# Kernel tuning notes

Hardware: AMD Instinct MI355X
Metric: run time of the kernel (lower is better)

The kernel has to match this reference:

```python
import jax, jax.numpy as jnp
import numpy as np

B, LQ, LK, D, H, DK, DV = 8, 1024, 1024, 512, 8, 64, 64
EPS = 1e-14          # K.epsilon()**2 with default K.epsilon()=1e-7
MASK_VALUE = -1e30   # default mask_value in call()


def setup_inputs() -> dict:
    key = jax.random.key(0)
    ks = jax.random.split(key, 7)
    query = jax.random.normal(ks[0], (B, LQ, D), jnp.float32)
    key_t = jax.random.normal(ks[1], (B, LK, D), jnp.float32)
    value = jax.random.normal(ks[2], (B, LK, D), jnp.float32)
    mask = jax.random.randint(ks[3], (B, LK), 0, 2).astype(jnp.float32)
    glorot = np.sqrt(2.0 / (D + DK)).astype(np.float32)
    Wq = jax.random.normal(ks[4], (H, D, DK), jnp.float32) * glorot
    Wk = jax.random.normal(ks[5], (H, D, DK), jnp.float32) * glorot
    Wv = jax.random.normal(ks[6], (H, D, DV), jnp.float32) * glorot
    gamma = jnp.ones((1,), jnp.float32)
    beta = jnp.zeros((1,), jnp.float32)
    return {"query": query, "key": key_t, "value": value, "mask": mask,
            "Wq": Wq, "Wk": Wk, "Wv": Wv, "gamma": gamma, "beta": beta}


def reference(query, key, value, mask, Wq, Wk, Wv, gamma, beta):
    # Per-head projections (the original's Python loop over heads, vectorized).
    q = jnp.einsum('bqd,hde->bhqe', query, Wq)   # [B,H,LQ,DK]
    k = jnp.einsum('bkd,hde->bhke', key, Wk)     # [B,H,LK,DK]
    v = jnp.einsum('bkd,hde->bhke', value, Wv)   # [B,H,LK,DV]
    # NOTE: no 1/sqrt(dk) scaling, faithful to the source.
    A = jnp.einsum('bhqe,bhke->bhqk', q, k)      # [B,H,LQ,LK]
    m = mask[:, None, None, :]                    # [B,1,1,LK] broadcast over heads & queries
    A = m * A + (1.0 - m) * MASK_VALUE
    A = jax.nn.softmax(A, axis=-1)
    o = jnp.einsum('bhqk,bhke->bhqe', A, v)      # [B,H,LQ,DV]
    conc = o.transpose(0, 2, 1, 3).reshape(B, LQ, H * DV)  # concat heads
    # Scalar-affine layernorm over the concatenated feature dim.
    mean = jnp.mean(conc, axis=-1, keepdims=True)
    var = jnp.mean(jnp.square(conc - mean), axis=-1, keepdims=True)
    x = (conc - mean) / jnp.sqrt(var + EPS)
    return x * gamma[0] + beta[0]
```

## Files before the change

### kernel.cpp

```cpp
#include <hip/hip_runtime.h>
#include <math.h>

#define NB 8
#define NLQ 1024
#define NLK 1024
#define ND 512
#define NH 8
#define MASKV -1e30f
#define LOG2E 1.44269504088896f
#define SHIFT2 32.0f

typedef unsigned short ushort_t;
typedef __attribute__((ext_vector_type(8))) _Float16 f16x8;
typedef __attribute__((ext_vector_type(8))) short bf16x8;
typedef __attribute__((ext_vector_type(16))) float f32x16;

__device__ __forceinline__ ushort_t f2h_bits(float f) {
    union { _Float16 h; ushort_t u; } v; v.h = (_Float16)f;
    return v.u;
}
__device__ __forceinline__ ushort_t f2bf(float f) {
    union { float f; unsigned u; } v; v.f = f;
    unsigned r = v.u + 0x7fffu + ((v.u >> 16) & 1u);
    return (ushort_t)(r >> 16);
}
__device__ __forceinline__ void gload16(const ushort_t* g, ushort_t* l) {
    __builtin_amdgcn_global_load_lds(
        (const __attribute__((address_space(1))) void*)g,
        (__attribute__((address_space(3))) void*)l, 16, 0, 0);
}
__device__ __forceinline__ void gload16f(const float* g, float* l) {
    __builtin_amdgcn_global_load_lds(
        (const __attribute__((address_space(1))) void*)g,
        (__attribute__((address_space(3))) void*)l, 16, 0, 0);
}
__device__ __forceinline__ unsigned pack_bf16_trunc(float p0, float p1) {
    return __builtin_amdgcn_perm(__float_as_uint(p1), __float_as_uint(p0),
                                 0x07060302u);
}

__global__ __launch_bounds__(256) void wsplit_kernel(
    const float* __restrict__ Wq, const float* __restrict__ Wk, const float* __restrict__ Wv,
    ushort_t* __restrict__ oq, ushort_t* __restrict__ ok, ushort_t* __restrict__ ov) {
    __shared__ float T[64][65];
    const int d0 = blockIdx.x * 64;
    const int h  = blockIdx.y;
    const int t  = blockIdx.z;
    const float* W = (t == 0) ? Wq : (t == 1) ? Wk : Wv;
    ushort_t* oh = (t == 0) ? oq : (t == 1) ? ok : ov;
    const int tid = threadIdx.x;
#pragma unroll
    for (int i = 0; i < 4; i++) {
        int r = (tid >> 4) + i * 16;
        int c = (tid & 15) * 4;
        float4 v = *(const float4*)&W[((size_t)h * ND + d0 + r) * 64 + c];
        *(float4*)&T[r][c] = v;
    }
    __syncthreads();
    const int e = tid & 63;
    const int dg = tid >> 6;
    ushort_t hs[16];
#pragma unroll
    for (int dd = 0; dd < 16; dd++) hs[dd] = f2h_bits(T[dg * 16 + dd][e]);
    size_t base = ((size_t)h * 64 + e) * ND + d0 + dg * 16;
#pragma unroll
    for (int c = 0; c < 2; c++) {
        uint4 wh;
        wh.x = (unsigned)hs[8*c+0] | ((unsigned)hs[8*c+1] << 16);
        wh.y = (unsigned)hs[8*c+2] | ((unsigned)hs[8*c+3] << 16);
        wh.z = (unsigned)hs[8*c+4] | ((unsigned)hs[8*c+5] << 16);
        wh.w = (unsigned)hs[8*c+6] | ((unsigned)hs[8*c+7] << 16);
        *(uint4*)&oh[base + 8 * c] = wh;
    }
}

__global__ __launch_bounds__(256, 3) void proj_mfma_kernel(
    const float* __restrict__ Xq, const float* __restrict__ Xk,
    const float* __restrict__ Xv, const ushort_t* __restrict__ Wbase,
    ushort_t* __restrict__ Obase) {
    __shared__ float    sXf[2][4160];
    __shared__ ushort_t sW [2][4160];

    const int l0 = blockIdx.x * 64;
    const int h  = blockIdx.y;
    const int z  = blockIdx.z;
    const int t  = z >> 3;
    const int b  = z & 7;
    const int tid  = threadIdx.x;
    const int wave = tid >> 6;
    const int lane = tid & 63;
    const int l31  = lane & 31;
    const int hib  = lane >> 5;
    const size_t bh = (size_t)b * NH + h;

    const float* Xt = (t == 0) ? Xq : (t == 1) ? Xk : Xv;
    const float* gx = Xt + ((size_t)b * NLQ + l0) * ND;
    const ushort_t* gw = Wbase + (size_t)t * ((size_t)NH * 64 * ND)
                       + (size_t)h * 64 * ND;
    ushort_t* out = Obase + (size_t)t * ((size_t)NB * NH * NLQ * 64);

    const int srow = lane >> 3;
    const int schk = (lane & 7) ^ srow;
    const int xrow = lane >> 4;
    const int xc16 = lane & 15;

    auto stage = [&](int buf, int d0) {
#pragma unroll
        for (int j = 0; j < 4; j++) {
            int s = j * 4 + wave;
            int row = s * 4 + xrow;
            int c16 = xc16 ^ ((row & 7) << 1);
            gload16f(gx + (size_t)row * ND + d0 + c16 * 4, sXf[buf] + s * 260);
        }
#pragma unroll
        for (int i = 0; i < 2; i++) {
            int u = i * 4 + wave;
            int row = u * 8 + srow;
            gload16(gw + (size_t)row * ND + d0 + schk * 8, sW[buf] + u * 520);
        }
    };

    f32x16 acc;
#pragma unroll
    for (int i = 0; i < 16; i++) acc[i] = 0.f;

    const int arow  = (wave >> 1) * 32 + l31;
    const int brow  = (wave & 1) * 32 + l31;
    const int xbase = (arow >> 2) * 260 + (arow & 3) * 64;
    const int sxz   = (arow & 7) << 1;
    const int bpad  = (brow >> 3) * 520 + (brow & 7) * 64;
    const int sw    = l31 & 7;

    stage(0, 0);
    int cur = 0;
#pragma unroll
    for (int kc = 0; kc < 8; kc++) {
        if (kc < 7) {
            stage(cur ^ 1, (kc + 1) * 64);
            asm volatile("s_waitcnt vmcnt(6)" ::: "memory");
        } else {
            asm volatile("s_waitcnt vmcnt(0)" ::: "memory");
        }
        __builtin_amdgcn_sched_barrier(0);
        __builtin_amdgcn_s_barrier();
        __builtin_amdgcn_sched_barrier(0);
#pragma unroll
        for (int c = 0; c < 4; c++) {
            const int sl = ((2 * c + hib) * 2) ^ sxz;
            const float* xp = &sXf[cur][xbase + sl * 4];
            float4 fa = *(const float4*)xp;
            float4 fb = *(const float4*)(xp + 4);
            f16x8 xh;
            xh[0] = (_Float16)fa.x; xh[1] = (_Float16)fa.y;
            xh[2] = (_Float16)fa.z; xh[3] = (_Float16)fa.w;
            xh[4] = (_Float16)fb.x; xh[5] = (_Float16)fb.y;
            xh[6] = (_Float16)fb.z; xh[7] = (_Float16)fb.w;
            const int pc = ((2 * c + hib) ^ sw) * 8;
            f16x8 wh = *(const f16x8*)&sW[cur][bpad + pc];
            acc = __builtin_amdgcn_mfma_f32_32x32x16_f16(xh, wh, acc, 0, 0, 0);
        }
        __builtin_amdgcn_sched_barrier(0);
        __builtin_amdgcn_s_barrier();
        __builtin_amdgcn_sched_barrier(0);
        cur ^= 1;
    }

    if (t < 2) {
        const float scale = (t == 0) ? LOG2E : 1.f;
        const size_t obase = (bh * NLQ + l0) * 64;
        const int e = (wave & 1) * 32 + l31;
#pragma unroll
        for (int r = 0; r < 16; r++) {
            int l = (wave >> 1) * 32 + (r & 3) + 8 * (r >> 2) + 4 * hib;
            out[obase + (size_t)l * 64 + e] = f2h_bits(acc[r] * scale);
        }
    } else {
        ushort_t (*T)[68] = (ushort_t(*)[68])sXf;
        const int e = (wave & 1) * 32 + l31;
#pragma unroll
        for (int r = 0; r < 16; r++) {
            int l = (wave >> 1) * 32 + (r & 3) + 8 * (r >> 2) + 4 * hib;
            T[e][l] = f2bf(acc[r]);
        }
        __syncthreads();
        const int e2 = tid >> 2;
        const int lc = (tid & 3) * 16;
        size_t base = (bh * 64 + e2) * NLK + l0 + lc;
        *(uint4*)&out[base]     = *(const uint4*)&T[e2][lc];
        *(uint4*)&out[base + 8] = *(const uint4*)&T[e2][lc + 8];
    }
}

__global__ __launch_bounds__(256, 4) void attn_kernel(
    const ushort_t* __restrict__ Qf, const ushort_t* __restrict__ Kf,
    const ushort_t* __restrict__ Vt, const float* __restrict__ maskp,
    float* __restrict__ Op) {
    __shared__ ushort_t sK[2][4160];
    __shared__ ushort_t sV[2][4160];
    __shared__ float sBias[1024];

    const int idx = blockIdx.x;
    const int bh_i = idx & 63;
    const int qc  = idx >> 6;
    const int b = bh_i >> 3, h = bh_i & 7;
    const size_t bh = (size_t)b * NH + h;

    const int tid  = threadIdx.x;
    const int wave = tid >> 6;
    const int lane = tid & 63;
    const int l31  = lane & 31;
    const int hib  = lane >> 5;
    const int q = qc * 128 + wave * 32 + l31;
    const int sw = l31 & 7;

    {
        const float* mrow = maskp + ((size_t)b << 10);
        float4 m0 = *(const float4*)&mrow[tid * 4];
        float4 bi;
        bi.x = (m0.x > 0.5f) ? -SHIFT2 : MASKV;
        bi.y = (m0.y > 0.5f) ? -SHIFT2 : MASKV;
        bi.z = (m0.z > 0.5f) ? -SHIFT2 : MASKV;
        bi.w = (m0.w > 0.5f) ? -SHIFT2 : MASKV;
        *(float4*)&sBias[tid * 4] = bi;
    }

    f16x8 qh[4];
    {
        const ushort_t* ph = Qf + (bh * NLQ + q) * 64 + hib * 8;
#pragma unroll
        for (int c = 0; c < 4; c++) qh[c] = *(const f16x8*)(ph + c * 16);
    }

    const int srow = lane >> 3;
    const int schk = (lane & 7) ^ srow;

    auto stage = [&](int buf, int k0) {
#pragma unroll
        for (int n = 0; n < 4; n++) {
            int u = wave + n * 4;
            if (u < 8) {
                int row = u * 8 + srow;
                int key = (row & ~12) | ((row & 4) << 1) | ((row & 8) >> 1);
                gload16(Kf + ((bh << 10) + k0 + key) * 64 + schk * 8,
                        sK[buf] + u * 520);
            } else {
                int u8 = u - 8;
                int row = u8 * 8 + srow;
                gload16(Vt + ((bh << 6) + row) * NLK + k0 + schk * 8,
                        sV[buf] + u8 * 520);
            }
        }
    };

    f32x16 O0, O1;
#pragma unroll
    for (int i = 0; i < 16; i++) { O0[i] = 0.f; O1[i] = 0.f; }
    float lrun = 0.f;

    const int rp0 = (l31 >> 3) * 520 + (l31 & 7) * 64;
    const int rp1 = rp0 + 4 * 520;

    stage(0, 0);
    __syncthreads();
    int cur = 0;

    for (int t = 0; t < 16; t++) {
        const int k0 = t << 6;
        if (t < 15) stage(cur ^ 1, k0 + 64);

        f32x16 S0, S1;
#pragma unroll
        for (int g = 0; g < 4; g++) {
            const int kb = k0 + 16 * (g >> 1) + 8 * hib + 4 * (g & 1);
            float4 b0 = *(const float4*)&sBias[kb];
            float4 b1 = *(const float4*)&sBias[kb + 32];
            S0[4 * g + 0] = b0.x; S0[4 * g + 1] = b0.y;
            S0[4 * g + 2] = b0.z; S0[4 * g + 3] = b0.w;
            S1[4 * g + 0] = b1.x; S1[4 * g + 1] = b1.y;
            S1[4 * g + 2] = b1.z; S1[4 * g + 3] = b1.w;
        }
#pragma unroll
        for (int c = 0; c < 4; c++) {
            const int pc = ((2 * c + hib) ^ sw) * 8;
            f16x8 a0 = *(const f16x8*)&sK[cur][rp0 + pc];
            f16x8 a1 = *(const f16x8*)&sK[cur][rp1 + pc];
            S0 = __builtin_amdgcn_mfma_f32_32x32x16_f16(a0, qh[c], S0, 0, 0, 0);
            S1 = __builtin_amdgcn_mfma_f32_32x32x16_f16(a1, qh[c], S1, 0, 0, 0);
        }

        unsigned pq[8][2];
#pragma unroll
        for (int g = 0; g < 8; g++) {
            float p0, p1, p2, p3;
            if (g < 4) {
                p0 = __builtin_amdgcn_exp2f(S0[4*g+0]);
                p1 = __builtin_amdgcn_exp2f(S0[4*g+1]);
                p2 = __builtin_amdgcn_exp2f(S0[4*g+2]);
                p3 = __builtin_amdgcn_exp2f(S0[4*g+3]);
            } else {
                p0 = __builtin_amdgcn_exp2f(S1[4*(g-4)+0]);
                p1 = __builtin_amdgcn_exp2f(S1[4*(g-4)+1]);
                p2 = __builtin_amdgcn_exp2f(S1[4*(g-4)+2]);
                p3 = __builtin_amdgcn_exp2f(S1[4*(g-4)+3]);
            }
            lrun += (p0 + p1) + (p2 + p3);
            pq[g][0] = pack_bf16_trunc(p0, p1);
            pq[g][1] = pack_bf16_trunc(p2, p3);
        }

#pragma unroll
        for (int c = 0; c < 4; c++) {
            union { unsigned u[4]; bf16x8 v; } pf;
            pf.u[0] = pq[2 * c][0];     pf.u[1] = pq[2 * c][1];
            pf.u[2] = pq[2 * c + 1][0]; pf.u[3] = pq[2 * c + 1][1];
            const int pc = ((2 * c + hib) ^ sw) * 8;
            bf16x8 v0 = *(const bf16x8*)&sV[cur][rp0 + pc];
            bf16x8 v1 = *(const bf16x8*)&sV[cur][rp1 + pc];
            O0 = __builtin_amdgcn_mfma_f32_32x32x16_bf16(v0, pf.v, O0, 0, 0, 0);
            O1 = __builtin_amdgcn_mfma_f32_32x32x16_bf16(v1, pf.v, O1, 0, 0, 0);
        }
        __syncthreads();
        cur ^= 1;
    }

    lrun += __shfl_xor(lrun, 32);
    const float linv = 1.f / lrun;
    float* obase = Op + ((size_t)(b * NLQ + q)) * (NH * 64) + h * 64;
#pragma unroll
    for (int me = 0; me < 2; me++) {
#pragma unroll
        for (int g = 0; g < 4; g++) {
            int e0 = me * 32 + 8 * g + 4 * hib;
            float4 o;
            if (me == 0) {
                o.x = O0[4 * g + 0] * linv; o.y = O0[4 * g + 1] * linv;
                o.z = O0[4 * g + 2] * linv; o.w = O0[4 * g + 3] * linv;
            } else {
                o.x = O1[4 * g + 0] * linv; o.y = O1[4 * g + 1] * linv;
                o.z = O1[4 * g + 2] * linv; o.w = O1[4 * g + 3] * linv;
            }
            *(float4*)&obase[e0] = o;
        }
    }
}

__global__ __launch_bounds__(256) void ln_kernel(const float* __restrict__ X,
                                                 const float* __restrict__ gamma,
                                                 const float* __restrict__ beta,
                                                 float* __restrict__ out) {
    const int row = blockIdx.x * 4 + (threadIdx.x >> 6);
    const int lane = threadIdx.x & 63;
    const float* x = &X[(size_t)row * 512];
    float4 v0 = *(const float4*)&x[lane * 8];
    float4 v1 = *(const float4*)&x[lane * 8 + 4];
    float sum = v0.x + v0.y + v0.z + v0.w + v1.x + v1.y + v1.z + v1.w;
    float sq = v0.x * v0.x + v0.y * v0.y + v0.z * v0.z + v0.w * v0.w
             + v1.x * v1.x + v1.y * v1.y + v1.z * v1.z + v1.w * v1.w;
#pragma unroll
    for (int off = 32; off > 0; off >>= 1) {
        sum += __shfl_down(sum, off);
        sq  += __shfl_down(sq, off);
    }
    sum = __shfl(sum, 0);
    sq  = __shfl(sq, 0);
    const float mean = sum * (1.f / 512.f);
    const float var = sq * (1.f / 512.f) - mean * mean;
    const float rstd = rsqrtf(var + 1e-14f);
    const float g = gamma[0], be = beta[0];
    float* o = &out[(size_t)row * 512];
    float4 r0, r1;
    r0.x = (v0.x - mean) * rstd * g + be;  r0.y = (v0.y - mean) * rstd * g + be;
    r0.z = (v0.z - mean) * rstd * g + be;  r0.w = (v0.w - mean) * rstd * g + be;
    r1.x = (v1.x - mean) * rstd * g + be;  r1.y = (v1.y - mean) * rstd * g + be;
    r1.z = (v1.z - mean) * rstd * g + be;  r1.w = (v1.w - mean) * rstd * g + be;
    *(float4*)&o[lane * 8] = r0;
    *(float4*)&o[lane * 8 + 4] = r1;
}

extern "C" void kernel_launch(void* const* d_in, const int* in_sizes, int n_in,
                              void* d_out, int out_size, void* d_ws, size_t ws_size,
                              hipStream_t stream) {
    const float* query = (const float*)d_in[0];
    const float* key_t = (const float*)d_in[1];
    const float* value = (const float*)d_in[2];
    const float* mask  = (const float*)d_in[3];
    const float* Wq    = (const float*)d_in[4];
    const float* Wk    = (const float*)d_in[5];
    const float* Wv    = (const float*)d_in[6];
    const float* gamma = (const float*)d_in[7];
    const float* beta  = (const float*)d_in[8];
    float* out = (float*)d_out;

    const size_t A = (size_t)NB * NLQ * ND;
    const size_t WS = (size_t)NH * 64 * ND;
    ushort_t* Qf = (ushort_t*)d_ws;
    ushort_t* Kf = Qf + A;
    ushort_t* Vt = Qf + 2 * A;
    ushort_t* Wt = Qf + 3 * A;

    wsplit_kernel<<<dim3(ND / 64, NH, 3), 256, 0, stream>>>(
        Wq, Wk, Wv, Wt, Wt + WS, Wt + 2 * WS);

    proj_mfma_kernel<<<dim3(NLQ / 64, NH, 24), 256, 0, stream>>>(
        query, key_t, value, Wt, Qf);

    attn_kernel<<<512, 256, 0, stream>>>(Qf, Kf, Vt, mask, out);

    ln_kernel<<<(NB * NLQ) / 4, 256, 0, stream>>>(out, gamma, beta, out);
}
```

Baseline: 184.9 us.

## Enlarge projection GEMM tiles to 128x128 and convert X to fp16 before LDS

The projection kernel now computes 128x128 output tiles (128 rows of one batch by two heads) with four 32x32 MFMA accumulators per wave, instead of one 64x64 tile per head. X is read into registers as fp32, converted to fp16 once, and written to LDS, where the old code staged fp32 in LDS and converted on every MFMA operand read. Weights are still staged asynchronously into LDS. The intent is to read X fewer times per head, halve LDS traffic for X, and raise MFMA density. In exchange there are more registers, occupancy drops to 2 blocks per CU, and the grid shrinks to 768 blocks.

```diff
diff --git a/kernel.cpp b/kernel.cpp
--- a/kernel.cpp
+++ b/kernel.cpp
@@ -25,11 +25,6 @@
     return (ushort_t)(r >> 16);
 }
 __device__ __forceinline__ void gload16(const ushort_t* g, ushort_t* l) {
-    __builtin_amdgcn_global_load_lds(
-        (const __attribute__((address_space(1))) void*)g,
-        (__attribute__((address_space(3))) void*)l, 16, 0, 0);
-}
-__device__ __forceinline__ void gload16f(const float* g, float* l) {
     __builtin_amdgcn_global_load_lds(
         (const __attribute__((address_space(1))) void*)g,
         (__attribute__((address_space(3))) void*)l, 16, 0, 0);
@@ -74,120 +69,172 @@
     }
 }
 
-__global__ __launch_bounds__(256, 3) void proj_mfma_kernel(
+__global__ __launch_bounds__(256, 2) void proj_gemm_kernel(
     const float* __restrict__ Xq, const float* __restrict__ Xk,
     const float* __restrict__ Xv, const ushort_t* __restrict__ Wbase,
     ushort_t* __restrict__ Obase) {
-    __shared__ float    sXf[2][4160];
-    __shared__ ushort_t sW [2][4160];
-
-    const int l0 = blockIdx.x * 64;
-    const int h  = blockIdx.y;
-    const int z  = blockIdx.z;
-    const int t  = z >> 3;
-    const int b  = z & 7;
+    __shared__ ushort_t sA[2][8320];
+    __shared__ ushort_t sB[2][8320];
+
+    const int bid   = blockIdx.x;
+    const int y     = bid / 192;
+    const int mglob = bid % 192;
+    const int t  = mglob >> 6;
+    const int b  = (mglob >> 3) & 7;
+    const int l0 = (mglob & 7) * 128;
+
     const int tid  = threadIdx.x;
     const int wave = tid >> 6;
     const int lane = tid & 63;
     const int l31  = lane & 31;
     const int hib  = lane >> 5;
-    const size_t bh = (size_t)b * NH + h;
+    const int wr = wave >> 1, wc = wave & 1;
 
     const float* Xt = (t == 0) ? Xq : (t == 1) ? Xk : Xv;
     const float* gx = Xt + ((size_t)b * NLQ + l0) * ND;
-    const ushort_t* gw = Wbase + (size_t)t * ((size_t)NH * 64 * ND)
-                       + (size_t)h * 64 * ND;
+    const ushort_t* gwt = Wbase + (size_t)t * ((size_t)NH * 64 * ND)
+                        + (size_t)y * 128 * ND;
     ushort_t* out = Obase + (size_t)t * ((size_t)NB * NH * NLQ * 64);
 
     const int srow = lane >> 3;
     const int schk = (lane & 7) ^ srow;
-    const int xrow = lane >> 4;
-    const int xc16 = lane & 15;
-
-    auto stage = [&](int buf, int d0) {
+
+    float4 ax[4][2];
+    auto aload = [&](int d0) {
 #pragma unroll
         for (int j = 0; j < 4; j++) {
-            int s = j * 4 + wave;
-            int row = s * 4 + xrow;
-            int c16 = xc16 ^ ((row & 7) << 1);
-            gload16f(gx + (size_t)row * ND + d0 + c16 * 4, sXf[buf] + s * 260);
-        }
-#pragma unroll
-        for (int i = 0; i < 2; i++) {
-            int u = i * 4 + wave;
+            int row = (j * 4 + wave) * 8 + srow;
+            const float* p = gx + (size_t)row * ND + d0 + schk * 8;
+            ax[j][0] = *(const float4*)p;
+            ax[j][1] = *(const float4*)(p + 4);
+        }
+    };
+    auto awrite = [&](int buf) {
+#pragma unroll
+        for (int j = 0; j < 4; j++) {
+            int u = j * 4 + wave;
+            uint4 hv;
+            hv.x = (unsigned)f2h_bits(ax[j][0].x) | ((unsigned)f2h_bits(ax[j][0].y) << 16);
+            hv.y = (unsigned)f2h_bits(ax[j][0].z) | ((unsigned)f2h_bits(ax[j][0].w) << 16);
+            hv.z = (unsigned)f2h_bits(ax[j][1].x) | ((unsigned)f2h_bits(ax[j][1].y) << 16);
+            hv.w = (unsigned)f2h_bits(ax[j][1].z) | ((unsigned)f2h_bits(ax[j][1].w) << 16);
+            *(uint4*)(sA[buf] + u * 520 + lane * 8) = hv;
+        }
+    };
+    auto bstage = [&](int buf, int d0) {
+#pragma unroll
+        for (int j = 0; j < 4; j++) {
+            int u = j * 4 + wave;
             int row = u * 8 + srow;
-            gload16(gw + (size_t)row * ND + d0 + schk * 8, sW[buf] + u * 520);
+            gload16(gwt + (size_t)row * ND + d0 + schk * 8, sB[buf] + u * 520);
         }
     };
 
-    f32x16 acc;
-#pragma unroll
-    for (int i = 0; i < 16; i++) acc[i] = 0.f;
-
-    const int arow  = (wave >> 1) * 32 + l31;
-    const int brow  = (wave & 1) * 32 + l31;
-    const int xbase = (arow >> 2) * 260 + (arow & 3) * 64;
-    const int sxz   = (arow & 7) << 1;
-    const int bpad  = (brow >> 3) * 520 + (brow & 7) * 64;
-    const int sw    = l31 & 7;
-
-    stage(0, 0);
+    f32x16 acc00, acc01, acc10, acc11;
+#pragma unroll
+    for (int i = 0; i < 16; i++) { acc00[i] = 0.f; acc01[i] = 0.f;
+                                   acc10[i] = 0.f; acc11[i] = 0.f; }
+
+    const int ga  = wr * 8 + (l31 >> 3);
+    const int gb  = wc * 8 + (l31 >> 3);
+    const int ro  = (l31 & 7) * 64;
+    const int swz = l31 & 7;
+
+    auto mfma_chunk = [&](int buf) {
+#pragma unroll
+        for (int c = 0; c < 4; c++) {
+            const int pc = ((2 * c + hib) ^ swz) * 8;
+            f16x8 a0 = *(const f16x8*)&sA[buf][ga * 520 + ro + pc];
+            f16x8 a1 = *(const f16x8*)&sA[buf][(ga + 4) * 520 + ro + pc];
+            f16x8 b0 = *(const f16x8*)&sB[buf][gb * 520 + ro + pc];
+            f16x8 b1 = *(const f16x8*)&sB[buf][(gb + 4) * 520 + ro + pc];
+            acc00 = __builtin_amdgcn_mfma_f32_32x32x16_f16(a0, b0, acc00, 0, 0, 0);
+            acc01 = __builtin_amdgcn_mfma_f32_32x32x16_f16(a0, b1, acc01, 0, 0, 0);
+            acc10 = __builtin_amdgcn_mfma_f32_32x32x16_f16(a1, b0, acc10, 0, 0, 0);
+            acc11 = __builtin_amdgcn_mfma_f32_32x32x16_f16(a1, b1, acc11, 0, 0, 0);
+        }
+    };
+
+    aload(0);
+    bstage(0, 0);
+    asm volatile("s_waitcnt vmcnt(4)" ::: "memory");
+    __builtin_amdgcn_sched_barrier(0);
+    awrite(0);
+    aload(64);
+    asm volatile("s_waitcnt vmcnt(8)" ::: "memory");
+    asm volatile("s_waitcnt lgkmcnt(0)" ::: "memory");
+    __builtin_amdgcn_sched_barrier(0);
+    __builtin_amdgcn_s_barrier();
+
     int cur = 0;
 #pragma unroll
     for (int kc = 0; kc < 8; kc++) {
         if (kc < 7) {
-            stage(cur ^ 1, (kc + 1) * 64);
-            asm volatile("s_waitcnt vmcnt(6)" ::: "memory");
+            bstage(cur ^ 1, (kc + 1) * 64);
+            mfma_chunk(cur);
+            asm volatile("s_waitcnt vmcnt(4)" ::: "memory");
+            __builtin_amdgcn_sched_barrier(0);
+            awrite(cur ^ 1);
+            if (kc < 6) {
+                aload((kc + 2) * 64);
+                asm volatile("s_waitcnt vmcnt(8)" ::: "memory");
+            } else {
+                asm volatile("s_waitcnt vmcnt(0)" ::: "memory");
+            }
+            asm volatile("s_waitcnt lgkmcnt(0)" ::: "memory");
+            __builtin_amdgcn_sched_barrier(0);
+            __builtin_amdgcn_s_barrier();
         } else {
-            asm volatile("s_waitcnt vmcnt(0)" ::: "memory");
-        }
-        __builtin_amdgcn_sched_barrier(0);
-        __builtin_amdgcn_s_barrier();
-        __builtin_amdgcn_sched_barrier(0);
-#pragma unroll
-        for (int c = 0; c < 4; c++) {
-            const int sl = ((2 * c + hib) * 2) ^ sxz;
-            const float* xp = &sXf[cur][xbase + sl * 4];
-            float4 fa = *(const float4*)xp;
-            float4 fb = *(const float4*)(xp + 4);
-            f16x8 xh;
-            xh[0] = (_Float16)fa.x; xh[1] = (_Float16)fa.y;
-            xh[2] = (_Float16)fa.z; xh[3] = (_Float16)fa.w;
-            xh[4] = (_Float16)fb.x; xh[5] = (_Float16)fb.y;
-            xh[6] = (_Float16)fb.z; xh[7] = (_Float16)fb.w;
-            const int pc = ((2 * c + hib) ^ sw) * 8;
-            f16x8 wh = *(const f16x8*)&sW[cur][bpad + pc];
-            acc = __builtin_amdgcn_mfma_f32_32x32x16_f16(xh, wh, acc, 0, 0, 0);
-        }
-        __builtin_amdgcn_sched_barrier(0);
-        __builtin_amdgcn_s_barrier();
-        __builtin_amdgcn_sched_barrier(0);
+            mfma_chunk(cur);
+        }
         cur ^= 1;
     }
 
     if (t < 2) {
         const float scale = (t == 0) ? LOG2E : 1.f;
-        const size_t obase = (bh * NLQ + l0) * 64;
-        const int e = (wave & 1) * 32 + l31;
-#pragma unroll
-        for (int r = 0; r < 16; r++) {
-            int l = (wave >> 1) * 32 + (r & 3) + 8 * (r >> 2) + 4 * hib;
-            out[obase + (size_t)l * 64 + e] = f2h_bits(acc[r] * scale);
+#pragma unroll
+        for (int mi = 0; mi < 2; mi++) {
+#pragma unroll
+            for (int ni = 0; ni < 2; ni++) {
+                const f32x16& a = (mi == 0) ? (ni == 0 ? acc00 : acc01)
+                                            : (ni == 0 ? acc10 : acc11);
+                int nglob = y * 128 + wc * 64 + ni * 32 + l31;
+                int hh = nglob >> 6, e = nglob & 63;
+                size_t obase = (((size_t)b * NH + hh) * NLQ + l0) * 64 + e;
+#pragma unroll
+                for (int r = 0; r < 16; r++) {
+                    int l = wr * 64 + mi * 32 + (r & 3) + 8 * (r >> 2) + 4 * hib;
+                    out[obase + (size_t)l * 64] = f2h_bits(a[r] * scale);
+                }
+            }
         }
     } else {
-        ushort_t (*T)[68] = (ushort_t(*)[68])sXf;
-        const int e = (wave & 1) * 32 + l31;
-#pragma unroll
-        for (int r = 0; r < 16; r++) {
-            int l = (wave >> 1) * 32 + (r & 3) + 8 * (r >> 2) + 4 * hib;
-            T[e][l] = f2bf(acc[r]);
-        }
         __syncthreads();
-        const int e2 = tid >> 2;
-        const int lc = (tid & 3) * 16;
-        size_t base = (bh * 64 + e2) * NLK + l0 + lc;
-        *(uint4*)&out[base]     = *(const uint4*)&T[e2][lc];
-        *(uint4*)&out[base + 8] = *(const uint4*)&T[e2][lc + 8];
+        ushort_t (*T)[130] = (ushort_t(*)[130])sA;
+#pragma unroll
+        for (int mi = 0; mi < 2; mi++) {
+#pragma unroll
+            for (int ni = 0; ni < 2; ni++) {
+                const f32x16& a = (mi == 0) ? (ni == 0 ? acc00 : acc01)
+                                            : (ni == 0 ? acc10 : acc11);
+                int n_loc = wc * 64 + ni * 32 + l31;
+#pragma unroll
+                for (int r = 0; r < 16; r++) {
+                    int l = wr * 64 + mi * 32 + (r & 3) + 8 * (r >> 2) + 4 * hib;
+                    T[n_loc][l] = f2bf(a[r]);
+                }
+            }
+        }
+        __syncthreads();
+        const int n_loc = tid >> 1;
+        const int half  = tid & 1;
+        const int hh = n_loc >> 6, e = n_loc & 63;
+        size_t obase = (((size_t)b * NH + y * 2 + hh) * 64 + e) * NLK
+                     + l0 + half * 64;
+        const ushort_t* src = &T[n_loc][half * 64];
+#pragma unroll
+        for (int c2 = 0; c2 < 8; c2++)
+            *(uint4*)&out[obase + c2 * 8] = *(const uint4*)&src[c2 * 8];
     }
 }
 
@@ -401,7 +448,7 @@
     wsplit_kernel<<<dim3(ND / 64, NH, 3), 256, 0, stream>>>(
         Wq, Wk, Wv, Wt, Wt + WS, Wt + 2 * WS);
 
-    proj_mfma_kernel<<<dim3(NLQ / 64, NH, 24), 256, 0, stream>>>(
+    proj_gemm_kernel<<<768, 256, 0, stream>>>(
         query, key_t, value, Wt, Qf);
 
     attn_kernel<<<512, 256, 0, stream>>>(Qf, Kf, Vt, mask, out);
```

Result: faster. 165.4 us (-10.5%).
